# Optimization experiments

Measured on AMD Instinct MI355X. Metric: run time of the kernel, lower is better.

Reference implementation:

```python
import jax, jax.numpy as jnp
import numpy as np

HIDDEN = 1024
HEADS = 16
HEAD_DIM = HIDDEN // HEADS


def setup_inputs() -> dict:
    key = jax.random.key(0)
    ks = jax.random.split(key, 9)
    B, S = 2, 2048
    std = 1.0 / np.sqrt(HIDDEN)
    inp = {
        'hidden_states': jax.random.normal(ks[0], (B, S, HIDDEN), dtype=jnp.float32),
        'attention_mask': jnp.ones((B, S), dtype=jnp.int32),
        'wq': jax.random.normal(ks[1], (HIDDEN, HIDDEN), dtype=jnp.float32) * std,
        'bq': jnp.zeros((HIDDEN,), dtype=jnp.float32),
        'wk': jax.random.normal(ks[2], (HIDDEN, HIDDEN), dtype=jnp.float32) * std,
        'bk': jnp.zeros((HIDDEN,), dtype=jnp.float32),
        'wv': jax.random.normal(ks[3], (HIDDEN, HIDDEN), dtype=jnp.float32) * std,
        'bv': jnp.zeros((HIDDEN,), dtype=jnp.float32),
        'wo': jax.random.normal(ks[4], (HIDDEN, HIDDEN), dtype=jnp.float32) * std,
        'bo': jnp.zeros((HIDDEN,), dtype=jnp.float32),
    }
    return inp


def reference(hidden_states, attention_mask, wq, bq, wk, bk, wv, bv, wo, bo):
    B, S, H = hidden_states.shape
    def heads(x):  # [B,S,H] -> [B,nh,S,hd]
        return x.reshape(B, S, HEADS, HEAD_DIM).transpose(0, 2, 1, 3)
    q = heads(hidden_states @ wq + bq)
    k = heads(hidden_states @ wk + bk)
    v = heads(hidden_states @ wv + bv)
    scores = jnp.einsum('bhqd,bhkd->bhqk', q, k) / np.sqrt(HEAD_DIM).astype(np.float32)
    causal = jnp.tril(jnp.ones((S, S), dtype=bool))  # True = keep
    keep = causal[None, None] & (attention_mask[:, None, None, :] != 0)
    scores = jnp.where(keep, scores, -jnp.inf)
    probs = jax.nn.softmax(scores, axis=-1)
    out = jnp.einsum('bhqk,bhkd->bhqd', probs, v)  # [B,nh,S,hd]
    out = out.transpose(0, 2, 1, 3).reshape(B, S, H)
    return out @ wo + bo
```

## Files before the change

### kernel.cpp

```cpp
#include <hip/hip_runtime.h>

#define HID   1024
#define SLEN  2048
#define NHEAD 16
#define HDIM  64
#define SC2L  0.18033688f

typedef unsigned short u16;
typedef _Float16 f16;
using bf16x8 = __attribute__((ext_vector_type(8))) short;
using h16x2  = __attribute__((ext_vector_type(2))) __fp16;
using f16x4  = __attribute__((ext_vector_type(4))) f16;
using f32x4  = __attribute__((ext_vector_type(4))) float;

typedef __attribute__((address_space(1))) void gvoid;
typedef __attribute__((address_space(3))) void lvoid;

__device__ __forceinline__ u16 f2bf(float f) {
  union { float f; unsigned u; } v; v.f = f;
  unsigned u = v.u;
  return (u16)((u + 0x7fffu + ((u >> 16) & 1u)) >> 16);
}

__device__ __forceinline__ void async_ld16(const u16* g, u16* l) {
  __builtin_amdgcn_global_load_lds((gvoid*)g, (lvoid*)l, 16, 0, 0);
}

__global__ __launch_bounds__(256) void prep_kernel(const float* __restrict__ x,
                                                   const float* __restrict__ wq,
                                                   const float* __restrict__ wk,
                                                   const float* __restrict__ wv,
                                                   const float* __restrict__ wo,
                                                   u16* __restrict__ xb,
                                                   u16* __restrict__ wt) {
  const int tid = threadIdx.x;
  if (blockIdx.z == 4) {
    const int bid = blockIdx.y * 32 + blockIdx.x;
#pragma unroll
    for (int it = 0; it < 4; ++it) {
      const int i = bid * 1024 + it * 256 + tid;
      float4 v = ((const float4*)x)[i];
      ushort4 o;
      o.x = f2bf(v.x); o.y = f2bf(v.y); o.z = f2bf(v.z); o.w = f2bf(v.w);
      ((ushort4*)xb)[i] = o;
    }
    return;
  }
  const float* src = (blockIdx.z == 0) ? wq : (blockIdx.z == 1) ? wk
                   : (blockIdx.z == 2) ? wv : wo;
  u16* dst = wt + (size_t)blockIdx.z * (HID * HID);
  __shared__ float tile[32][33];
  const int n0 = blockIdx.x * 32, k0 = blockIdx.y * 32;
  const int xx = tid & 31, yy = tid >> 5;
  for (int i = yy; i < 32; i += 8)
    tile[i][xx] = src[(size_t)(k0 + i) * HID + n0 + xx];
  __syncthreads();
  for (int i = yy; i < 32; i += 8)
    dst[(size_t)(n0 + i) * HID + k0 + xx] = f2bf(tile[xx][i]);
}

__global__ __launch_bounds__(256) void gemm_qkv_kernel(const u16* __restrict__ A,
                                                       const u16* __restrict__ Bt,
                                                       const float* __restrict__ bq,
                                                       const float* __restrict__ bk,
                                                       const float* __restrict__ bv,
                                                       u16* __restrict__ Qb,
                                                       u16* __restrict__ Kb,
                                                       u16* __restrict__ VTf) {
  __shared__ u16 smem[16384];
  const int tid  = threadIdx.x;
  const int wave = tid >> 6, lane = tid & 63;
  const int quad = lane >> 4, l16 = lane & 15;
  const int n0g = blockIdx.x * 128;
  const int region = blockIdx.x >> 3;
  const int colbase = (blockIdx.x & 7) * 128;
  const int m0 = blockIdx.y * 128;
  const int wm = (wave & 1) * 64, wn = (wave >> 1) * 64;

  f32x4 acc[4][4] = {};
  const int srow = lane >> 2;
  const int scol = (lane & 3) * 8;

#define STAGE_G(kt, bi)                                                          \
  for (int c = wave; c < 8; c += 4) {                                            \
    async_ld16(A  + (size_t)(m0  + c * 16 + srow) * HID + (kt) + scol,           \
               &smem[(bi) * 8192 + c * 512]);                                    \
    async_ld16(Bt + (size_t)(n0g + c * 16 + srow) * HID + (kt) + scol,           \
               &smem[(bi) * 8192 + 4096 + c * 512]);                             \
  }

  STAGE_G(0, 0);
  for (int ks = 0; ks < 32; ++ks) {
    const int bi = ks & 1;
    if (ks < 31) {
      STAGE_G((ks + 1) * 32, bi ^ 1);
      asm volatile("s_waitcnt vmcnt(4)" ::: "memory");
    } else {
      asm volatile("s_waitcnt vmcnt(0)" ::: "memory");
    }
    __builtin_amdgcn_s_barrier();

    const u16* sA = smem + bi * 8192;
    const u16* sB = smem + bi * 8192 + 4096;
    bf16x8 af[4], bfr[4];
#pragma unroll
    for (int t = 0; t < 4; ++t) {
      af[t]  = *(const bf16x8*)&sA[(wm + t * 16 + l16) * 32 + quad * 8];
      bfr[t] = *(const bf16x8*)&sB[(wn + t * 16 + l16) * 32 + quad * 8];
    }
#pragma unroll
    for (int mt = 0; mt < 4; ++mt)
#pragma unroll
      for (int nt = 0; nt < 4; ++nt)
        acc[mt][nt] = __builtin_amdgcn_mfma_f32_16x16x32_bf16(af[mt], bfr[nt],
                                                              acc[mt][nt], 0, 0, 0);
    __builtin_amdgcn_s_barrier();
  }
#undef STAGE_G

  const float* bias = (region == 0) ? bq : (region == 1) ? bk : bv;
  float bvv[4];
#pragma unroll
  for (int nt = 0; nt < 4; ++nt) bvv[nt] = bias[colbase + wn + nt * 16 + l16];

  if (region == 2) {
    const int bb = m0 >> 11;
    const int m0loc = m0 & 2047;
    const int h0 = colbase >> 6;
    u16* T = smem;
#pragma unroll
    for (int h2 = 0; h2 < 2; ++h2) {
      __syncthreads();
      if ((wave >> 1) == h2) {
#pragma unroll
        for (int mt = 0; mt < 4; ++mt)
#pragma unroll
          for (int nt = 0; nt < 4; ++nt)
#pragma unroll
            for (int r = 0; r < 4; ++r) {
              const int sl = (wave & 1) * 64 + mt * 16 + quad * 4 + r;
              const int dl = nt * 16 + l16;
              union { f16 h; u16 u; } cv;
              cv.h = (f16)(acc[mt][nt][r] + bvv[nt]);
              T[dl * 128 + (((sl >> 3) ^ l16) * 8) + (sl & 7)] = cv.u;
            }
      }
      __syncthreads();
      const int d = tid >> 2, sg = (tid & 3) * 4;
      u16* slab0 = VTf + ((size_t)((bb * NHEAD + h0 + h2) * 128 + (m0loc >> 4))) * 1024;
#pragma unroll
      for (int cc = 0; cc < 4; ++cc) {
        const int cl = sg + cc;
        const int ph = cl ^ (d & 15);
        const int slot = (d * 2 + (cl & 1)) ^ ((d >> 2) & 1);
        *(bf16x8*)(slab0 + (size_t)(cl >> 1) * 1024 + slot * 8)
            = *(const bf16x8*)&T[d * 128 + ph * 8];
      }
    }
    return;
  }

  u16* C = (region == 0) ? Qb : Kb;
#pragma unroll
  for (int mt = 0; mt < 4; ++mt)
#pragma unroll
    for (int r = 0; r < 4; ++r) {
      const int row = m0 + wm + mt * 16 + quad * 4 + r;
#pragma unroll
      for (int nt = 0; nt < 4; ++nt) {
        const int col = colbase + wn + nt * 16 + l16;
        C[(size_t)row * HID + col] = f2bf(acc[mt][nt][r] + bvv[nt]);
      }
    }
}

__global__ __launch_bounds__(256) void gemm_o_kernel(const u16* __restrict__ A,
                                                     const u16* __restrict__ Bt,
                                                     const float* __restrict__ bias,
                                                     float* __restrict__ Cf) {
  __shared__ u16 smem[12288];
  const int tid  = threadIdx.x;
  const int wave = tid >> 6, lane = tid & 63;
  const int quad = lane >> 4, l16 = lane & 15;
  const int n0 = blockIdx.x * 128;
  const int m0 = blockIdx.y * 64;
  const int wn = wave * 32;

  f32x4 acc[4][2] = {};
  const int srow = lane >> 2;
  const int scol = (lane & 3) * 8;

#define STAGE_O(kt, bi)                                                          \
  for (int c = wave; c < 12; c += 4) {                                           \
    if (c < 4) async_ld16(A + (size_t)(m0 + c * 16 + srow) * HID + (kt) + scol,  \
                          &smem[(bi) * 6144 + c * 512]);                         \
    else async_ld16(Bt + (size_t)(n0 + (c - 4) * 16 + srow) * HID + (kt) + scol, \
                    &smem[(bi) * 6144 + 2048 + (c - 4) * 512]);                  \
  }

  STAGE_O(0, 0);
  for (int ks = 0; ks < 32; ++ks) {
    const int bi = ks & 1;
    if (ks < 31) {
      STAGE_O((ks + 1) * 32, bi ^ 1);
      asm volatile("s_waitcnt vmcnt(3)" ::: "memory");
    } else {
      asm volatile("s_waitcnt vmcnt(0)" ::: "memory");
    }
    __builtin_amdgcn_s_barrier();

    const u16* sA = smem + bi * 6144;
    const u16* sB = smem + bi * 6144 + 2048;
    bf16x8 af[4], bfr[2];
#pragma unroll
    for (int t = 0; t < 4; ++t)
      af[t] = *(const bf16x8*)&sA[(t * 16 + l16) * 32 + quad * 8];
#pragma unroll
    for (int t = 0; t < 2; ++t)
      bfr[t] = *(const bf16x8*)&sB[(wn + t * 16 + l16) * 32 + quad * 8];
#pragma unroll
    for (int mt = 0; mt < 4; ++mt)
#pragma unroll
      for (int nt = 0; nt < 2; ++nt)
        acc[mt][nt] = __builtin_amdgcn_mfma_f32_16x16x32_bf16(af[mt], bfr[nt],
                                                              acc[mt][nt], 0, 0, 0);
    __builtin_amdgcn_s_barrier();
  }
#undef STAGE_O

  float bvv[2];
#pragma unroll
  for (int nt = 0; nt < 2; ++nt) bvv[nt] = bias[n0 + wn + nt * 16 + l16];
#pragma unroll
  for (int mt = 0; mt < 4; ++mt)
#pragma unroll
    for (int r = 0; r < 4; ++r) {
      const int row = m0 + mt * 16 + quad * 4 + r;
#pragma unroll
      for (int nt = 0; nt < 2; ++nt)
        Cf[(size_t)row * HID + n0 + wn + nt * 16 + l16] = acc[mt][nt][r] + bvv[nt];
    }
}

__global__ __launch_bounds__(256, 2) void flash_attn_kernel(const u16* __restrict__ Q,
                                                            const u16* __restrict__ K,
                                                            const u16* __restrict__ VT,
                                                            const int* __restrict__ mask,
                                                            u16* __restrict__ O) {
  const int xb = blockIdx.x, h = blockIdx.y, b = blockIdx.z;
  const int tid  = threadIdx.x;
  const int wave = tid >> 6, lane = tid & 63;
  const int quad = lane >> 4, l16 = lane & 15;

  __shared__ alignas(16) char smraw[35840];
  u16*   Ks  = (u16*)smraw;
  u16*   Vt  = (u16*)(smraw + 16384);
  float* Ob0 = (float*)smraw;
  float* Ob1 = (float*)(smraw + 16896);
  float* lb  = (float*)(smraw + 33792);

  const u16* Kh  = K  + (size_t)b * SLEN * HID + h * HDIM;
  const u16* Vth = VT + (size_t)(b * NHEAD + h) * (128 * 1024);

  const int srow8 = lane >> 3;
  const int gch   = (lane & 7) ^ srow8;
  const int rx    = l16 & 7;

  unsigned mw = 0;
  {
    const int4* mrow = (const int4*)(mask + b * SLEN);
#pragma unroll
    for (int c = 0; c < 8; ++c) {
      int4 m = mrow[lane * 8 + c];
      mw |= (m.x ? 1u : 0u) << (c * 4);
      mw |= (m.y ? 1u : 0u) << (c * 4 + 1);
      mw |= (m.z ? 1u : 0u) << (c * 4 + 2);
      mw |= (m.w ? 1u : 0u) << (c * 4 + 3);
    }
  }
  const int mb = (wave & 1) * 16 + quad * 4;

  const int r0s = wave * 16 + srow8;
#define STAGE_KV(jt, bufi)                                                      \
  {                                                                             \
    u16* kd = Ks + (bufi) * 4096 + wave * 1024;                                 \
    async_ld16(Kh + (size_t)((jt) * 64 + r0s) * HID + gch * 8,       kd);       \
    async_ld16(Kh + (size_t)((jt) * 64 + r0s + 8) * HID + gch * 8,   kd + 512); \
    const u16* vs = Vth + (size_t)((jt) * 4 + wave) * 1024;                     \
    u16* vd = Vt + (bufi) * 4096 + wave * 1024;                                 \
    async_ld16(vs + lane * 8,        vd);                                       \
    async_ld16(vs + (64 + lane) * 8, vd + 512);                                 \
  }

  for (int phase = 0; phase < 2; ++phase) {
    const int qt = phase ? (31 - xb) : xb;
    const int q0 = qt * 64;

    bf16x8 qb[4][2];
#pragma unroll
    for (int nt = 0; nt < 4; ++nt) {
      const u16* qp = Q + (size_t)(b * SLEN + q0 + nt * 16 + l16) * HID + h * HDIM + quad * 8;
      qb[nt][0] = *(const bf16x8*)qp;
      qb[nt][1] = *(const bf16x8*)(qp + 32);
    }

    f32x4 oacc[4][4] = {};
    float l_part[4] = {0.f, 0.f, 0.f, 0.f};

    STAGE_KV(0, 0);

    for (int j = 0; j <= qt; ++j) {
      const int buf = j & 1;
      u16* KsB = Ks + buf * 4096;
      u16* VtB = Vt + buf * 4096;

      if (j < qt) {
        STAGE_KV(j + 1, buf ^ 1);
        asm volatile("s_waitcnt vmcnt(6)" ::: "memory");
      } else {
        asm volatile("s_waitcnt vmcnt(2)" ::: "memory");
      }

      const unsigned wbits = __shfl(mw, 2 * j + (wave >> 1));
      float map[4];
#pragma unroll
      for (int r = 0; r < 4; ++r)
        map[r] = ((wbits >> (mb + r)) & 1u) ? 0.f : -1e30f;

      const u16* kp = KsB + (wave * 16 + l16) * 64;
      const int ph0 = quad ^ rx;
      const bf16x8 ka0 = *(const bf16x8*)(kp + ph0 * 8);
      const bf16x8 ka1 = *(const bf16x8*)(kp + (ph0 ^ 4) * 8);

      float p[4][4];
      __builtin_amdgcn_s_setprio(1);
#pragma unroll
      for (int nt = 0; nt < 4; ++nt) {
        f32x4 z = {0.f, 0.f, 0.f, 0.f};
        z = __builtin_amdgcn_mfma_f32_16x16x32_bf16(ka0, qb[nt][0], z, 0, 0, 0);
        z = __builtin_amdgcn_mfma_f32_16x16x32_bf16(ka1, qb[nt][1], z, 0, 0, 0);
#pragma unroll
        for (int r = 0; r < 4; ++r)
          p[nt][r] = exp2f(fmaf(z[r], SC2L, map[r]));
      }
      __builtin_amdgcn_s_setprio(0);
      if (j == qt) {
#pragma unroll
        for (int nt = 0; nt < 4; ++nt)
#pragma unroll
          for (int r = 0; r < 4; ++r)
            if (wave * 16 + quad * 4 + r > nt * 16 + l16) p[nt][r] = 0.f;
      }

      f16x4 pb[4];
#pragma unroll
      for (int nt = 0; nt < 4; ++nt) {
        l_part[nt] += (p[nt][0] + p[nt][1]) + (p[nt][2] + p[nt][3]);
        union { h16x2 h[2]; f16x4 v; } u;
        u.h[0] = __builtin_amdgcn_cvt_pkrtz(p[nt][0], p[nt][1]);
        u.h[1] = __builtin_amdgcn_cvt_pkrtz(p[nt][2], p[nt][3]);
        pb[nt] = u.v;
      }

      if (j < qt) {
        asm volatile("s_waitcnt vmcnt(4)" ::: "memory");
      } else {
        asm volatile("s_waitcnt vmcnt(0)" ::: "memory");
      }

      __builtin_amdgcn_s_setprio(1);
#pragma unroll
      for (int dt = 0; dt < 4; ++dt) {
        const int dd = dt * 16 + l16;
        const int slot = (dd * 2 + (quad >> 1)) ^ ((dd >> 2) & 1);
        const f16x4 va = *(const f16x4*)(VtB + wave * 1024 + slot * 8 + (quad & 1) * 4);
#pragma unroll
        for (int nt = 0; nt < 4; ++nt)
          oacc[dt][nt] = __builtin_amdgcn_mfma_f32_16x16x16f16(va, pb[nt], oacc[dt][nt], 0, 0, 0);
      }
      __builtin_amdgcn_s_setprio(0);
    }

    __syncthreads();

#pragma unroll
    for (int nt = 0; nt < 4; ++nt) {
      l_part[nt] += __shfl_xor(l_part[nt], 16);
      l_part[nt] += __shfl_xor(l_part[nt], 32);
    }
    if (quad == 0)
#pragma unroll
      for (int nt = 0; nt < 4; ++nt) lb[wave * 64 + nt * 16 + l16] = l_part[nt];

    if ((wave & 1) == 0) {
      float* ob = (wave == 0) ? Ob0 : Ob1;
#pragma unroll
      for (int dt = 0; dt < 4; ++dt)
#pragma unroll
        for (int nt = 0; nt < 4; ++nt)
#pragma unroll
          for (int r = 0; r < 4; ++r)
            ob[(dt * 16 + quad * 4 + r) * 66 + nt * 16 + l16] = oacc[dt][nt][r];
    }
    __syncthreads();
    if (wave & 1) {
      float* ob = (wave == 1) ? Ob0 : Ob1;
#pragma unroll
      for (int dt = 0; dt < 4; ++dt)
#pragma unroll
        for (int nt = 0; nt < 4; ++nt)
#pragma unroll
          for (int r = 0; r < 4; ++r)
            ob[(dt * 16 + quad * 4 + r) * 66 + nt * 16 + l16] += oacc[dt][nt][r];
    }
    __syncthreads();

    {
      const int q  = tid >> 2;
      const int dc = tid & 3;
      const float l = lb[q] + lb[64 + q] + lb[128 + q] + lb[192 + q];
      const float inv = 1.f / l;
      u16 ob[16];
#pragma unroll
      for (int e = 0; e < 16; ++e) {
        const int d = dc * 16 + e;
        ob[e] = f2bf((Ob0[d * 66 + q] + Ob1[d * 66 + q]) * inv);
      }
      u16* op = O + (size_t)(b * SLEN + q0 + q) * HID + h * HDIM + dc * 16;
      *(bf16x8*)op       = *(bf16x8*)&ob[0];
      *(bf16x8*)(op + 8) = *(bf16x8*)&ob[8];
    }
    __syncthreads();
  }
#undef STAGE_KV
}

extern "C" void kernel_launch(void* const* d_in, const int* in_sizes, int n_in,
                              void* d_out, int out_size, void* d_ws, size_t ws_size,
                              hipStream_t stream) {
  const float* x    = (const float*)d_in[0];
  const int*   mask = (const int*)d_in[1];
  const float* wq   = (const float*)d_in[2];
  const float* bq   = (const float*)d_in[3];
  const float* wk   = (const float*)d_in[4];
  const float* bk   = (const float*)d_in[5];
  const float* wv   = (const float*)d_in[6];
  const float* bv   = (const float*)d_in[7];
  const float* wo   = (const float*)d_in[8];
  const float* bo   = (const float*)d_in[9];
  float* out = (float*)d_out;

  char* ws = (char*)d_ws;
  u16* XBF = (u16*)(ws);
  u16* WT  = (u16*)(ws + (8u  << 20));
  u16* QBF = (u16*)(ws + (16u << 20));
  u16* KBF = (u16*)(ws + (24u << 20));
  u16* VTF = (u16*)(ws + (32u << 20));
  u16* ATT = (u16*)(ws);

  prep_kernel<<<dim3(32, 32, 5), 256, 0, stream>>>(x, wq, wk, wv, wo, XBF, WT);
  gemm_qkv_kernel<<<dim3(24, 32), 256, 0, stream>>>(XBF, WT, bq, bk, bv, QBF, KBF, VTF);
  flash_attn_kernel<<<dim3(16, NHEAD, 2), 256, 0, stream>>>(QBF, KBF, VTF, mask, ATT);
  gemm_o_kernel<<<dim3(8, 64), 256, 0, stream>>>(ATT, WT + (3u << 20), bo, out);
}
```

Baseline: 198.3 us.

## Split causal attention into one block per query tile and remap GEMM block order

The flash attention kernel previously processed two paired query tiles per block in sequence. It now launches 1024 blocks, each handling one query tile, with a 1D index that interleaves heavy and light tiles and groups heads by XCD-style striding. Both GEMM kernels remap their block index so consecutive hardware slots land on different XCDs, aiming for better L2 locality. The s_setprio hints in the attention loop are removed. More blocks means more per-block setup such as the mask load and epilogue, but gives finer-grained scheduling of the uneven causal work.

New measurement: 204.5 us. 3.2% more time.

```diff
diff --git a/kernel.cpp b/kernel.cpp
--- a/kernel.cpp
+++ b/kernel.cpp
@@ -71,10 +71,13 @@
   const int tid  = threadIdx.x;
   const int wave = tid >> 6, lane = tid & 63;
   const int quad = lane >> 4, l16 = lane & 15;
-  const int n0g = blockIdx.x * 128;
-  const int region = blockIdx.x >> 3;
-  const int colbase = (blockIdx.x & 7) * 128;
-  const int m0 = blockIdx.y * 128;
+  const int raw = blockIdx.y * 24 + blockIdx.x;
+  const int logi = (raw & 7) * 96 + (raw >> 3);
+  const int bx = logi % 24, by = logi / 24;
+  const int n0g = bx * 128;
+  const int region = bx >> 3;
+  const int colbase = (bx & 7) * 128;
+  const int m0 = by * 128;
   const int wm = (wave & 1) * 64, wn = (wave >> 1) * 64;
 
   f32x4 acc[4][4] = {};
@@ -182,8 +185,10 @@
   const int tid  = threadIdx.x;
   const int wave = tid >> 6, lane = tid & 63;
   const int quad = lane >> 4, l16 = lane & 15;
-  const int n0 = blockIdx.x * 128;
-  const int m0 = blockIdx.y * 64;
+  const int raw = blockIdx.y * 8 + blockIdx.x;
+  const int logi = (raw & 7) * 64 + (raw >> 3);
+  const int n0 = (logi & 7) * 128;
+  const int m0 = (logi >> 3) * 64;
   const int wn = wave * 32;
 
   f32x4 acc[4][2] = {};
@@ -247,7 +252,12 @@
                                                             const u16* __restrict__ VT,
                                                             const int* __restrict__ mask,
                                                             u16* __restrict__ O) {
-  const int xb = blockIdx.x, h = blockIdx.y, b = blockIdx.z;
+  const int id = blockIdx.x;
+  const int p  = id >> 1, s = id & 1;
+  const int hb = p & 31;
+  const int h  = hb & 15, b = hb >> 4;
+  const int qb = p >> 5;
+  const int qt = s ? qb : 31 - qb;
   const int tid  = threadIdx.x;
   const int wave = tid >> 6, lane = tid & 63;
   const int quad = lane >> 4, l16 = lane & 15;
@@ -279,6 +289,19 @@
     }
   }
   const int mb = (wave & 1) * 16 + quad * 4;
+
+  const int q0 = qt * 64;
+
+  bf16x8 qb_[4][2];
+#pragma unroll
+  for (int nt = 0; nt < 4; ++nt) {
+    const u16* qp = Q + (size_t)(b * SLEN + q0 + nt * 16 + l16) * HID + h * HDIM + quad * 8;
+    qb_[nt][0] = *(const bf16x8*)qp;
+    qb_[nt][1] = *(const bf16x8*)(qp + 32);
+  }
+
+  f32x4 oacc[4][4] = {};
+  float l_part[4] = {0.f, 0.f, 0.f, 0.f};
 
   const int r0s = wave * 16 + srow8;
 #define STAGE_KV(jt, bufi)                                                      \
@@ -292,147 +315,126 @@
     async_ld16(vs + (64 + lane) * 8, vd + 512);                                 \
   }
 
-  for (int phase = 0; phase < 2; ++phase) {
-    const int qt = phase ? (31 - xb) : xb;
-    const int q0 = qt * 64;
-
-    bf16x8 qb[4][2];
+  STAGE_KV(0, 0);
+
+  for (int j = 0; j <= qt; ++j) {
+    const int buf = j & 1;
+    u16* KsB = Ks + buf * 4096;
+    u16* VtB = Vt + buf * 4096;
+
+    if (j < qt) {
+      STAGE_KV(j + 1, buf ^ 1);
+      asm volatile("s_waitcnt vmcnt(6)" ::: "memory");
+    } else {
+      asm volatile("s_waitcnt vmcnt(2)" ::: "memory");
+    }
+
+    const unsigned wbits = __shfl(mw, 2 * j + (wave >> 1));
+    float map[4];
+#pragma unroll
+    for (int r = 0; r < 4; ++r)
+      map[r] = ((wbits >> (mb + r)) & 1u) ? 0.f : -1e30f;
+
+    const u16* kp = KsB + (wave * 16 + l16) * 64;
+    const int ph0 = quad ^ rx;
+    const bf16x8 ka0 = *(const bf16x8*)(kp + ph0 * 8);
+    const bf16x8 ka1 = *(const bf16x8*)(kp + (ph0 ^ 4) * 8);
+
+    float p_[4][4];
 #pragma unroll
     for (int nt = 0; nt < 4; ++nt) {
-      const u16* qp = Q + (size_t)(b * SLEN + q0 + nt * 16 + l16) * HID + h * HDIM + quad * 8;
-      qb[nt][0] = *(const bf16x8*)qp;
-      qb[nt][1] = *(const bf16x8*)(qp + 32);
-    }
-
-    f32x4 oacc[4][4] = {};
-    float l_part[4] = {0.f, 0.f, 0.f, 0.f};
-
-    STAGE_KV(0, 0);
-
-    for (int j = 0; j <= qt; ++j) {
-      const int buf = j & 1;
-      u16* KsB = Ks + buf * 4096;
-      u16* VtB = Vt + buf * 4096;
-
-      if (j < qt) {
-        STAGE_KV(j + 1, buf ^ 1);
-        asm volatile("s_waitcnt vmcnt(6)" ::: "memory");
-      } else {
-        asm volatile("s_waitcnt vmcnt(2)" ::: "memory");
-      }
-
-      const unsigned wbits = __shfl(mw, 2 * j + (wave >> 1));
-      float map[4];
+      f32x4 z = {0.f, 0.f, 0.f, 0.f};
+      z = __builtin_amdgcn_mfma_f32_16x16x32_bf16(ka0, qb_[nt][0], z, 0, 0, 0);
+      z = __builtin_amdgcn_mfma_f32_16x16x32_bf16(ka1, qb_[nt][1], z, 0, 0, 0);
 #pragma unroll
       for (int r = 0; r < 4; ++r)
-        map[r] = ((wbits >> (mb + r)) & 1u) ? 0.f : -1e30f;
-
-      const u16* kp = KsB + (wave * 16 + l16) * 64;
-      const int ph0 = quad ^ rx;
-      const bf16x8 ka0 = *(const bf16x8*)(kp + ph0 * 8);
-      const bf16x8 ka1 = *(const bf16x8*)(kp + (ph0 ^ 4) * 8);
-
-      float p[4][4];
-      __builtin_amdgcn_s_setprio(1);
-#pragma unroll
-      for (int nt = 0; nt < 4; ++nt) {
-        f32x4 z = {0.f, 0.f, 0.f, 0.f};
-        z = __builtin_amdgcn_mfma_f32_16x16x32_bf16(ka0, qb[nt][0], z, 0, 0, 0);
-        z = __builtin_amdgcn_mfma_f32_16x16x32_bf16(ka1, qb[nt][1], z, 0, 0, 0);
+        p_[nt][r] = exp2f(fmaf(z[r], SC2L, map[r]));
+    }
+    if (j == qt) {
+#pragma unroll
+      for (int nt = 0; nt < 4; ++nt)
 #pragma unroll
         for (int r = 0; r < 4; ++r)
-          p[nt][r] = exp2f(fmaf(z[r], SC2L, map[r]));
-      }
-      __builtin_amdgcn_s_setprio(0);
-      if (j == qt) {
-#pragma unroll
-        for (int nt = 0; nt < 4; ++nt)
-#pragma unroll
-          for (int r = 0; r < 4; ++r)
-            if (wave * 16 + quad * 4 + r > nt * 16 + l16) p[nt][r] = 0.f;
-      }
-
-      f16x4 pb[4];
-#pragma unroll
-      for (int nt = 0; nt < 4; ++nt) {
-        l_part[nt] += (p[nt][0] + p[nt][1]) + (p[nt][2] + p[nt][3]);
-        union { h16x2 h[2]; f16x4 v; } u;
-        u.h[0] = __builtin_amdgcn_cvt_pkrtz(p[nt][0], p[nt][1]);
-        u.h[1] = __builtin_amdgcn_cvt_pkrtz(p[nt][2], p[nt][3]);
-        pb[nt] = u.v;
-      }
-
-      if (j < qt) {
-        asm volatile("s_waitcnt vmcnt(4)" ::: "memory");
-      } else {
-        asm volatile("s_waitcnt vmcnt(0)" ::: "memory");
-      }
-
-      __builtin_amdgcn_s_setprio(1);
-#pragma unroll
-      for (int dt = 0; dt < 4; ++dt) {
-        const int dd = dt * 16 + l16;
-        const int slot = (dd * 2 + (quad >> 1)) ^ ((dd >> 2) & 1);
-        const f16x4 va = *(const f16x4*)(VtB + wave * 1024 + slot * 8 + (quad & 1) * 4);
-#pragma unroll
-        for (int nt = 0; nt < 4; ++nt)
-          oacc[dt][nt] = __builtin_amdgcn_mfma_f32_16x16x16f16(va, pb[nt], oacc[dt][nt], 0, 0, 0);
-      }
-      __builtin_amdgcn_s_setprio(0);
-    }
-
-    __syncthreads();
-
+          if (wave * 16 + quad * 4 + r > nt * 16 + l16) p_[nt][r] = 0.f;
+    }
+
+    f16x4 pb[4];
 #pragma unroll
     for (int nt = 0; nt < 4; ++nt) {
-      l_part[nt] += __shfl_xor(l_part[nt], 16);
-      l_part[nt] += __shfl_xor(l_part[nt], 32);
-    }
-    if (quad == 0)
-#pragma unroll
-      for (int nt = 0; nt < 4; ++nt) lb[wave * 64 + nt * 16 + l16] = l_part[nt];
-
-    if ((wave & 1) == 0) {
-      float* ob = (wave == 0) ? Ob0 : Ob1;
-#pragma unroll
-      for (int dt = 0; dt < 4; ++dt)
-#pragma unroll
-        for (int nt = 0; nt < 4; ++nt)
-#pragma unroll
-          for (int r = 0; r < 4; ++r)
-            ob[(dt * 16 + quad * 4 + r) * 66 + nt * 16 + l16] = oacc[dt][nt][r];
-    }
-    __syncthreads();
-    if (wave & 1) {
-      float* ob = (wave == 1) ? Ob0 : Ob1;
-#pragma unroll
-      for (int dt = 0; dt < 4; ++dt)
-#pragma unroll
-        for (int nt = 0; nt < 4; ++nt)
-#pragma unroll
-          for (int r = 0; r < 4; ++r)
-            ob[(dt * 16 + quad * 4 + r) * 66 + nt * 16 + l16] += oacc[dt][nt][r];
-    }
-    __syncthreads();
-
-    {
-      const int q  = tid >> 2;
-      const int dc = tid & 3;
-      const float l = lb[q] + lb[64 + q] + lb[128 + q] + lb[192 + q];
-      const float inv = 1.f / l;
-      u16 ob[16];
-#pragma unroll
-      for (int e = 0; e < 16; ++e) {
-        const int d = dc * 16 + e;
-        ob[e] = f2bf((Ob0[d * 66 + q] + Ob1[d * 66 + q]) * inv);
-      }
-      u16* op = O + (size_t)(b * SLEN + q0 + q) * HID + h * HDIM + dc * 16;
-      *(bf16x8*)op       = *(bf16x8*)&ob[0];
-      *(bf16x8*)(op + 8) = *(bf16x8*)&ob[8];
-    }
-    __syncthreads();
+      l_part[nt] += (p_[nt][0] + p_[nt][1]) + (p_[nt][2] + p_[nt][3]);
+      union { h16x2 h[2]; f16x4 v; } u;
+      u.h[0] = __builtin_amdgcn_cvt_pkrtz(p_[nt][0], p_[nt][1]);
+      u.h[1] = __builtin_amdgcn_cvt_pkrtz(p_[nt][2], p_[nt][3]);
+      pb[nt] = u.v;
+    }
+
+    if (j < qt) {
+      asm volatile("s_waitcnt vmcnt(4)" ::: "memory");
+    } else {
+      asm volatile("s_waitcnt vmcnt(0)" ::: "memory");
+    }
+
+#pragma unroll
+    for (int dt = 0; dt < 4; ++dt) {
+      const int dd = dt * 16 + l16;
+      const int slot = (dd * 2 + (quad >> 1)) ^ ((dd >> 2) & 1);
+      const f16x4 va = *(const f16x4*)(VtB + wave * 1024 + slot * 8 + (quad & 1) * 4);
+#pragma unroll
+      for (int nt = 0; nt < 4; ++nt)
+        oacc[dt][nt] = __builtin_amdgcn_mfma_f32_16x16x16f16(va, pb[nt], oacc[dt][nt], 0, 0, 0);
+    }
   }
 #undef STAGE_KV
+
+  __syncthreads();
+
+#pragma unroll
+  for (int nt = 0; nt < 4; ++nt) {
+    l_part[nt] += __shfl_xor(l_part[nt], 16);
+    l_part[nt] += __shfl_xor(l_part[nt], 32);
+  }
+  if (quad == 0)
+#pragma unroll
+    for (int nt = 0; nt < 4; ++nt) lb[wave * 64 + nt * 16 + l16] = l_part[nt];
+
+  if ((wave & 1) == 0) {
+    float* ob = (wave == 0) ? Ob0 : Ob1;
+#pragma unroll
+    for (int dt = 0; dt < 4; ++dt)
+#pragma unroll
+      for (int nt = 0; nt < 4; ++nt)
+#pragma unroll
+        for (int r = 0; r < 4; ++r)
+          ob[(dt * 16 + quad * 4 + r) * 66 + nt * 16 + l16] = oacc[dt][nt][r];
+  }
+  __syncthreads();
+  if (wave & 1) {
+    float* ob = (wave == 1) ? Ob0 : Ob1;
+#pragma unroll
+    for (int dt = 0; dt < 4; ++dt)
+#pragma unroll
+      for (int nt = 0; nt < 4; ++nt)
+#pragma unroll
+        for (int r = 0; r < 4; ++r)
+          ob[(dt * 16 + quad * 4 + r) * 66 + nt * 16 + l16] += oacc[dt][nt][r];
+  }
+  __syncthreads();
+
+  {
+    const int q  = tid >> 2;
+    const int dc = tid & 3;
+    const float l = lb[q] + lb[64 + q] + lb[128 + q] + lb[192 + q];
+    const float inv = 1.f / l;
+    u16 ob[16];
+#pragma unroll
+    for (int e = 0; e < 16; ++e) {
+      const int d = dc * 16 + e;
+      ob[e] = f2bf((Ob0[d * 66 + q] + Ob1[d * 66 + q]) * inv);
+    }
+    u16* op = O + (size_t)(b * SLEN + q0 + q) * HID + h * HDIM + dc * 16;
+    *(bf16x8*)op       = *(bf16x8*)&ob[0];
+    *(bf16x8*)(op + 8) = *(bf16x8*)&ob[8];
+  }
 }
 
 extern "C" void kernel_launch(void* const* d_in, const int* in_sizes, int n_in,
@@ -460,6 +462,6 @@
 
   prep_kernel<<<dim3(32, 32, 5), 256, 0, stream>>>(x, wq, wk, wv, wo, XBF, WT);
   gemm_qkv_kernel<<<dim3(24, 32), 256, 0, stream>>>(XBF, WT, bq, bk, bv, QBF, KBF, VTF);
-  flash_attn_kernel<<<dim3(16, NHEAD, 2), 256, 0, stream>>>(QBF, KBF, VTF, mask, ATT);
+  flash_attn_kernel<<<dim3(1024), 256, 0, stream>>>(QBF, KBF, VTF, mask, ATT);
   gemm_o_kernel<<<dim3(8, 64), 256, 0, stream>>>(ATT, WT + (3u << 20), bo, out);
 }
```
